# Kernel tuning notes

Measured on AMD Instinct MI355X. Metric: run time of the kernel, lower is better.

## Reference

```python
import jax, jax.numpy as jnp
import numpy as np

B, N, F_IN, F_OUT = 8, 8192, 64, 64
LN_EPS = 1e-5


def setup_inputs() -> dict:
    key = jax.random.key(0)
    k_x, k_adj, k_ws, k_wn = jax.random.split(key, 4)
    scale = 1.0 / np.sqrt(F_IN)
    return {
        "x": jax.random.normal(k_x, (B, N, F_IN), dtype=jnp.float32),
        "adj_matrix": jax.random.randint(k_adj, (N, N), 0, 2, dtype=jnp.int32),
        "W_self": jax.random.normal(k_ws, (F_IN, F_OUT), dtype=jnp.float32) * scale,
        "b_self": jnp.zeros((F_OUT,), dtype=jnp.float32),
        "W_neigh": jax.random.normal(k_wn, (F_IN, F_OUT), dtype=jnp.float32) * scale,
        "b_neigh": jnp.zeros((F_OUT,), dtype=jnp.float32),
        "ln_gamma": jnp.ones((F_OUT,), dtype=jnp.float32),
        "ln_beta": jnp.zeros((F_OUT,), dtype=jnp.float32),
    }


def reference(x, adj_matrix, W_self, b_self, W_neigh, b_neigh, ln_gamma, ln_beta):
    # GraphSAGE 'mean' conv (vectorized form of the per-node python loop):
    # agg[b,i,:] = mean over neighbors j (adj[i,j] > 0) of x[b,j,:]
    A = (adj_matrix > 0).astype(x.dtype)                 # [N, N]
    deg = A.sum(axis=1)                                  # [N]
    agg = jnp.einsum('ij,bjf->bif', A, x)                # [B, N, F_in]
    agg = agg / jnp.maximum(deg, 1.0)[None, :, None]
    neigh_out = agg @ W_neigh + b_neigh                  # [B, N, F_out]
    # nodes with no neighbors keep zeros (loop never writes them)
    neigh_out = jnp.where((deg > 0)[None, :, None], neigh_out, 0.0)
    self_out = x @ W_self + b_self                       # [B, N, F_out]
    out = jax.nn.relu(self_out + neigh_out)              # SAGE internal relu
    # GCNBlock: relu (idempotent here) -> LayerNorm; dropout is eval-mode identity
    out = jax.nn.relu(out)
    mu = out.mean(axis=-1, keepdims=True)
    var = jnp.mean((out - mu) ** 2, axis=-1, keepdims=True)
    out = (out - mu) * jax.lax.rsqrt(var + LN_EPS) * ln_gamma + ln_beta
    return out
```

## Files before the change

kernel.cpp:

```cpp
#include <hip/hip_runtime.h>

#define NN 8192

typedef __bf16 bf16x8 __attribute__((ext_vector_type(8)));
typedef float f32x4 __attribute__((ext_vector_type(4)));
typedef unsigned short u16x8 __attribute__((ext_vector_type(8)));
typedef int i32x4 __attribute__((ext_vector_type(4)));
typedef int i32x16 __attribute__((ext_vector_type(16)));

#define GLOBAL_AS __attribute__((address_space(1)))
#define LDS_AS __attribute__((address_space(3)))

__device__ __forceinline__ unsigned short f2bf(float f) {
  unsigned int u = __builtin_bit_cast(unsigned int, f);
  u += 0x7FFFu + ((u >> 16) & 1u);
  return (unsigned short)(u >> 16);
}
__device__ __forceinline__ float bf2f(unsigned short b) {
  unsigned int u = ((unsigned int)b) << 16;
  return __builtin_bit_cast(float, u);
}

__device__ __forceinline__ i32x4 expA(unsigned int h) {
  i32x4 a;
  a[0] = (int)((((h      ) & 0xFu) * 0x204081u) & 0x01010101u);
  a[1] = (int)((((h >> 4 ) & 0xFu) * 0x204081u) & 0x01010101u);
  a[2] = (int)((((h >> 8 ) & 0xFu) * 0x204081u) & 0x01010101u);
  a[3] = (int)((((h >> 12) & 0xFu) * 0x204081u) & 0x01010101u);
  return a;
}

__global__ __launch_bounds__(256) void packprep_kernel(
    const int* __restrict__ adj, unsigned long long* __restrict__ maskT,
    float* __restrict__ degp,
    const float* __restrict__ x, const float* __restrict__ Wself,
    const float* __restrict__ bself, const float* __restrict__ Wneigh,
    char* __restrict__ Yq, unsigned short* __restrict__ Sout) {
  __shared__ __align__(16) unsigned char xb[4][1024];
  __shared__ __align__(16) unsigned short xa[64 * 64];
  __shared__ __align__(16) unsigned short bm[128 * 64];

  if (blockIdx.x < 4096) {
    const int lane = threadIdx.x & 63;
    const int wv = threadIdx.x >> 6;
    const int bid = blockIdx.x;
    const int row = ((bid & 7) << 10) + ((bid >> 3) << 1) + (wv >> 1);
    const int half = wv & 1;
    const int* src = adj + (size_t)row * NN + half * 4096;
    unsigned int nib[16];
#pragma unroll
    for (int c = 0; c < 16; ++c) {
      int4 v = *(const int4*)(src + c * 256 + lane * 4);
      nib[c] = (unsigned int)(v.x > 0)
             | ((unsigned int)(v.y > 0) << 1)
             | ((unsigned int)(v.z > 0) << 2)
             | ((unsigned int)(v.w > 0) << 3);
    }
#pragma unroll
    for (int c = 0; c < 16; ++c) xb[wv][c * 64 + lane] = (unsigned char)nib[c];
    __syncthreads();
    uint4 B = *(const uint4*)&xb[wv][lane * 16];
    unsigned int t0 = (B.x | (B.x >> 4)) & 0x00FF00FFu; t0 = (t0 | (t0 >> 8)) & 0xFFFFu;
    unsigned int t1 = (B.y | (B.y >> 4)) & 0x00FF00FFu; t1 = (t1 | (t1 >> 8)) & 0xFFFFu;
    unsigned int t2 = (B.z | (B.z >> 4)) & 0x00FF00FFu; t2 = (t2 | (t2 >> 8)) & 0xFFFFu;
    unsigned int t3 = (B.w | (B.w >> 4)) & 0x00FF00FFu; t3 = (t3 | (t3 >> 8)) & 0xFFFFu;
    unsigned long long word = (unsigned long long)(t0 | (t1 << 16))
                            | ((unsigned long long)(t2 | (t3 << 16)) << 32);
    const size_t P = (size_t)((half << 5) + (lane >> 1));
    maskT[(P * NN + row) * 2 + (lane & 1)] = word;
    int deg = (int)__popcll(word);
#pragma unroll
    for (int m = 1; m < 64; m <<= 1) deg += __shfl_xor(deg, m);
    if (lane == 0) degp[half * NN + row] = (float)deg;
    return;
  }

  const int t = threadIdx.x;
  const int pb = blockIdx.x - 4096;
  const int b = pb >> 7;
  const int j0 = (pb & 127) << 6;

  {
    const float* Wsel = (t < 128) ? Wneigh : Wself;
    const int tt = t & 127;
    const int k = tt >> 1;
    const int c0 = (tt & 1) << 5;
    const int nbase = (t < 128) ? 0 : 64;
    const float4* src = (const float4*)(Wsel + k * 64 + c0);
#pragma unroll
    for (int q = 0; q < 8; ++q) {
      float4 v = src[q];
      int n0 = nbase + c0 + q * 4;
      int n;
      n = n0 + 0; bm[n * 64 + (k ^ ((n & 7) << 3))] = f2bf(v.x);
      n = n0 + 1; bm[n * 64 + (k ^ ((n & 7) << 3))] = f2bf(v.y);
      n = n0 + 2; bm[n * 64 + (k ^ ((n & 7) << 3))] = f2bf(v.z);
      n = n0 + 3; bm[n * 64 + (k ^ ((n & 7) << 3))] = f2bf(v.w);
    }
  }
  {
    const int j = t >> 2, q = t & 3;
    const float* xrow = x + ((size_t)b * NN + j0 + j) * 64 + q * 16;
    float4 v0 = *(const float4*)(xrow + 0);
    float4 v1 = *(const float4*)(xrow + 4);
    float4 v2 = *(const float4*)(xrow + 8);
    float4 v3 = *(const float4*)(xrow + 12);
    u16x8 p0, p1;
    p0[0] = f2bf(v0.x); p0[1] = f2bf(v0.y); p0[2] = f2bf(v0.z); p0[3] = f2bf(v0.w);
    p0[4] = f2bf(v1.x); p0[5] = f2bf(v1.y); p0[6] = f2bf(v1.z); p0[7] = f2bf(v1.w);
    p1[0] = f2bf(v2.x); p1[1] = f2bf(v2.y); p1[2] = f2bf(v2.z); p1[3] = f2bf(v2.w);
    p1[4] = f2bf(v3.x); p1[5] = f2bf(v3.y); p1[6] = f2bf(v3.z); p1[7] = f2bf(v3.w);
    const int base = q * 16;
    const int sw = (j & 7) << 3;
    *(u16x8*)&xa[j * 64 + (base ^ sw)] = p0;
    *(u16x8*)&xa[j * 64 + ((base + 8) ^ sw)] = p1;
  }
  __syncthreads();

  const int lane = t & 63, w = t >> 6;
  const int rl = lane & 15, hi = lane >> 4;
  f32x4 acc[8];
#pragma unroll
  for (int i = 0; i < 8; ++i) acc[i] = (f32x4){0.f, 0.f, 0.f, 0.f};

#pragma unroll
  for (int ks = 0; ks < 2; ++ks) {
    const int r = w * 16 + rl;
    const int kel = ks * 32 + hi * 8;
    bf16x8 af = __builtin_bit_cast(bf16x8, *(u16x8*)&xa[r * 64 + (kel ^ ((r & 7) << 3))]);
#pragma unroll
    for (int nf = 0; nf < 8; ++nf) {
      const int n = nf * 16 + rl;
      bf16x8 bv = __builtin_bit_cast(bf16x8, *(u16x8*)&bm[n * 64 + (kel ^ ((n & 7) << 3))]);
      acc[nf] = __builtin_amdgcn_mfma_f32_16x16x32_bf16(af, bv, acc[nf], 0, 0, 0);
    }
  }
#pragma unroll
  for (int nf = 0; nf < 8; ++nf) {
    if (nf < 4) {
      const int n = nf * 16 + rl;
      unsigned int pkt = 0;
#pragma unroll
      for (int r = 0; r < 4; ++r) {
        float v = fminf(fmaxf(acc[nf][r] * 16.0f, -127.0f), 127.0f);
        int iv = __float2int_rn(v);
        pkt |= ((unsigned int)(iv & 0xFF)) << (r * 8);
      }
      *(unsigned int*)(Yq + (size_t)(b * 64 + n) * NN + j0 + w * 16 + hi * 4) = pkt;
    } else {
      const int fo = (nf - 4) * 16 + rl;
      const float bsv = bself[fo];
#pragma unroll
      for (int r = 0; r < 4; ++r) {
        const int jj = w * 16 + hi * 4 + r;
        Sout[((size_t)b * NN + j0 + jj) * 64 + fo] = f2bf(acc[nf][r] + bsv);
      }
    }
  }
}

__global__ __launch_bounds__(256, 2) void gemm_kernel(
    const i32x4* __restrict__ mask,
    const char* __restrict__ Yq,
    unsigned short* __restrict__ Cp) {
  __shared__ __align__(16) char yL[8][8192];
  const int tid = threadIdx.x;
  const int lane = tid & 63, w = tid >> 6;
  const int nid = ((blockIdx.x & 7) << 6) + (blockIdx.x >> 3);
  const int ksp = nid >> 8;
  const int nb = (nid >> 5) & 7;
  const int mb = nid & 31;
  const int i0 = mb << 8;
  const int kbase = ksp << 12;
  const int ncol0 = nb << 6;
  const int l31 = lane & 31, l5 = lane >> 5;
  const int hs16 = l5 << 4;

  const int cst = (w << 4) + (lane >> 3);
  const char* ysrc = Yq + (size_t)(ncol0 + cst) * NN + kbase
                     + (((lane & 7) ^ (cst & 7)) << 4);
  const i32x4* mqT = mask + ((size_t)(ksp << 5)) * NN + i0 + (w << 6) + l31;

  int boff[2][4];
#pragma unroll
  for (int nf = 0; nf < 2; ++nf)
#pragma unroll
    for (int s = 0; s < 4; ++s) {
      const int col = (nf << 5) + l31;
      const int g = (s << 1) + l5;
      boff[nf][s] = (col << 7) + ((g ^ (col & 7)) << 4);
    }

  i32x16 acc[2][2];
#pragma unroll
  for (int mf = 0; mf < 2; ++mf)
#pragma unroll
    for (int nf = 0; nf < 2; ++nf)
#pragma unroll
      for (int e = 0; e < 16; ++e) acc[mf][nf][e] = 0;

#define BARRIER  __builtin_amdgcn_s_barrier()
#define MEMBAR   asm volatile("" ::: "memory")
#define WAIT_VM6 asm volatile("s_waitcnt vmcnt(6)" ::: "memory")

#define STAGE(t)                                                              \
  {                                                                           \
    __builtin_amdgcn_global_load_lds(                                         \
        (GLOBAL_AS void*)const_cast<char*>(ysrc + (size_t)((t) & 31) * 128),  \
        (LDS_AS void*)&yL[(t) & 7][w << 11], 16, 0, 0);                       \
    __builtin_amdgcn_global_load_lds(                                         \
        (GLOBAL_AS void*)const_cast<char*>(ysrc + (size_t)8 * NN              \
                                           + (size_t)((t) & 31) * 128),       \
        (LDS_AS void*)&yL[(t) & 7][(w << 11) + 1024], 16, 0, 0);              \
  }

#define LOADM(M0, M1, t)                                                      \
  { M0 = mqT[(size_t)((t) & 31) * NN]; M1 = mqT[(size_t)((t) & 31) * NN + 32]; }

#define COMPUTE(t, M0, M1)                                                    \
  {                                                                           \
    const char* yb_ = &yL[(t) & 7][0];                                        \
    __builtin_amdgcn_s_setprio(1);                                            \
    _Pragma("unroll")                                                         \
    for (int s_ = 0; s_ < 4; ++s_) {                                          \
      i32x4 b0_ = *(const i32x4*)(yb_ + boff[0][s_]);                         \
      i32x4 b1_ = *(const i32x4*)(yb_ + boff[1][s_]);                         \
      unsigned int h0_ = (unsigned int)(M0)[s_] >> hs16;                      \
      unsigned int h1_ = (unsigned int)(M1)[s_] >> hs16;                      \
      i32x4 a0_ = expA(h0_);                                                  \
      i32x4 a1_ = expA(h1_);                                                  \
      acc[0][0] = __builtin_amdgcn_mfma_i32_32x32x32_i8(a0_, b0_, acc[0][0], 0, 0, 0); \
      acc[0][1] = __builtin_amdgcn_mfma_i32_32x32x32_i8(a0_, b1_, acc[0][1], 0, 0, 0); \
      acc[1][0] = __builtin_amdgcn_mfma_i32_32x32x32_i8(a1_, b0_, acc[1][0], 0, 0, 0); \
      acc[1][1] = __builtin_amdgcn_mfma_i32_32x32x32_i8(a1_, b1_, acc[1][1], 0, 0, 0); \
    }                                                                         \
    __builtin_amdgcn_s_setprio(0);                                            \
  }

  i32x4 Ma0, Ma1, Mb0, Mb1;
  STAGE(0);
  STAGE(1);
  STAGE(2);
  LOADM(Ma0, Ma1, 0);

  for (int t2 = 0; t2 < 32; t2 += 2) {
    LOADM(Mb0, Mb1, t2 + 1);
    STAGE(t2 + 3);
    WAIT_VM6;
    BARRIER; MEMBAR;
    COMPUTE(t2, Ma0, Ma1);
    LOADM(Ma0, Ma1, t2 + 2);
    STAGE(t2 + 4);
    WAIT_VM6;
    BARRIER; MEMBAR;
    COMPUTE(t2 + 1, Mb0, Mb1);
  }
  asm volatile("s_waitcnt vmcnt(0)" ::: "memory");

#pragma unroll
  for (int mf = 0; mf < 2; ++mf)
#pragma unroll
    for (int nf = 0; nf < 2; ++nf) {
      const int col = ncol0 + (nf << 5) + l31;
#pragma unroll
      for (int r = 0; r < 16; ++r) {
        const int row = i0 + (w << 6) + (mf << 5) + (r & 3) + ((r >> 2) << 3) + (l5 << 2);
        Cp[((size_t)ksp * NN + row) * 512 + col] = f2bf((float)acc[mf][nf][r] * 0.0625f);
      }
    }
#undef BARRIER
#undef MEMBAR
#undef WAIT_VM6
#undef STAGE
#undef LOADM
#undef COMPUTE
}

__global__ __launch_bounds__(256) void epi_kernel(
    const unsigned short* __restrict__ Cp, const float* __restrict__ degp,
    const unsigned short* __restrict__ Sbf, const float* __restrict__ bneigh,
    const float* __restrict__ gamma, const float* __restrict__ beta,
    float* __restrict__ out) {
  const int lane = threadIdx.x & 63;
  const int wid = (blockIdx.x << 2) + (threadIdx.x >> 6);
  const int b = wid >> 13;
  const int i = wid & (NN - 1);
  const float deg = degp[i] + degp[NN + i];
  const float rdeg = 1.0f / fmaxf(deg, 1.0f);
  const size_t cidx = (size_t)i * 512 + b * 64 + lane;
  const float c = bf2f(Cp[cidx]) + bf2f(Cp[(size_t)NN * 512 + cidx]);
  const float sv = bf2f(Sbf[((size_t)b * NN + i) * 64 + lane]);
  float v = sv + ((deg > 0.5f) ? (c * rdeg + bneigh[lane]) : 0.0f);
  v = fmaxf(v, 0.0f);
  float s1 = v, s2 = v * v;
#pragma unroll
  for (int m = 1; m < 64; m <<= 1) {
    s1 += __shfl_xor(s1, m);
    s2 += __shfl_xor(s2, m);
  }
  const float mu = s1 * 0.015625f;
  const float var = s2 * 0.015625f - mu * mu;
  const float o = (v - mu) * rsqrtf(var + 1e-5f) * gamma[lane] + beta[lane];
  out[((size_t)b * NN + i) * 64 + lane] = o;
}

extern "C" void kernel_launch(void* const* d_in, const int* in_sizes, int n_in,
                              void* d_out, int out_size, void* d_ws, size_t ws_size,
                              hipStream_t stream) {
  (void)in_sizes; (void)n_in; (void)out_size; (void)ws_size;
  const float* x      = (const float*)d_in[0];
  const int*   adj    = (const int*)d_in[1];
  const float* Wself  = (const float*)d_in[2];
  const float* bself  = (const float*)d_in[3];
  const float* Wneigh = (const float*)d_in[4];
  const float* bneigh = (const float*)d_in[5];
  const float* gamma  = (const float*)d_in[6];
  const float* beta   = (const float*)d_in[7];
  char* ws = (char*)d_ws;
  char*               Yq    = ws;
  unsigned long long* maskT = (unsigned long long*)(ws + 4194304);
  unsigned short*     Sbf   = (unsigned short*)(ws + 12582912);
  unsigned short*     Cp    = (unsigned short*)(ws + 20971520);
  float*              degp  = (float*)(ws + 37748736);
  float*              out   = (float*)d_out;

  packprep_kernel<<<dim3(5120), dim3(256), 0, stream>>>(
      adj, maskT, degp, x, Wself, bself, Wneigh, Yq, Sbf);
  gemm_kernel<<<dim3(512), dim3(256), 0, stream>>>((const i32x4*)maskT, Yq, Cp);
  epi_kernel<<<dim3(16384), dim3(256), 0, stream>>>(Cp, degp, Sbf, bneigh, gamma, beta, out);
}
```

Measured before the change: 118.9 us.

## Split pack/prep kernels and retile int8 GEMM to smaller M tile with higher occupancy

Splits the fused pack+prep kernel into two separate launches and drops the block-wide barrier in the adjacency packing path, since each wave only reads its own LDS slice. The int8 MFMA GEMM is retiled from 256 to 128 rows per block, with half the accumulators per wave, a 4-deep LDS ring instead of 8, and launch bounds for 4 blocks per CU. The pipeline now issues the next stage after the barrier. The aim is higher occupancy and better latency hiding. In exchange, each Yq column tile is reloaded by twice as many blocks, and there is one extra kernel launch.

```diff
diff --git a/kernel.cpp b/kernel.cpp
--- a/kernel.cpp
+++ b/kernel.cpp
@@ -30,55 +30,49 @@
   return a;
 }
 
-__global__ __launch_bounds__(256) void packprep_kernel(
+__global__ __launch_bounds__(256) void pack_kernel(
     const int* __restrict__ adj, unsigned long long* __restrict__ maskT,
-    float* __restrict__ degp,
+    float* __restrict__ degp) {
+  __shared__ __align__(16) unsigned char xb[4][1024];
+  const int lane = threadIdx.x & 63;
+  const int wv = threadIdx.x >> 6;
+  const int bid = blockIdx.x;
+  const int row = ((bid & 7) << 10) + ((bid >> 3) << 1) + (wv >> 1);
+  const int half = wv & 1;
+  const int* src = adj + (size_t)row * NN + half * 4096;
+#pragma unroll
+  for (int c = 0; c < 16; ++c) {
+    int4 v = *(const int4*)(src + c * 256 + lane * 4);
+    unsigned int nib = (unsigned int)(v.x > 0)
+                     | ((unsigned int)(v.y > 0) << 1)
+                     | ((unsigned int)(v.z > 0) << 2)
+                     | ((unsigned int)(v.w > 0) << 3);
+    xb[wv][c * 64 + lane] = (unsigned char)nib;
+  }
+  uint4 B = *(const uint4*)&xb[wv][lane * 16];
+  unsigned int t0 = (B.x | (B.x >> 4)) & 0x00FF00FFu; t0 = (t0 | (t0 >> 8)) & 0xFFFFu;
+  unsigned int t1 = (B.y | (B.y >> 4)) & 0x00FF00FFu; t1 = (t1 | (t1 >> 8)) & 0xFFFFu;
+  unsigned int t2 = (B.z | (B.z >> 4)) & 0x00FF00FFu; t2 = (t2 | (t2 >> 8)) & 0xFFFFu;
+  unsigned int t3 = (B.w | (B.w >> 4)) & 0x00FF00FFu; t3 = (t3 | (t3 >> 8)) & 0xFFFFu;
+  unsigned long long word = (unsigned long long)(t0 | (t1 << 16))
+                          | ((unsigned long long)(t2 | (t3 << 16)) << 32);
+  const size_t P = (size_t)((half << 5) + (lane >> 1));
+  maskT[(P * NN + row) * 2 + (lane & 1)] = word;
+  int deg = (int)__popcll(word);
+#pragma unroll
+  for (int m = 1; m < 64; m <<= 1) deg += __shfl_xor(deg, m);
+  if (lane == 0) degp[half * NN + row] = (float)deg;
+}
+
+__global__ __launch_bounds__(256) void prep_kernel(
     const float* __restrict__ x, const float* __restrict__ Wself,
     const float* __restrict__ bself, const float* __restrict__ Wneigh,
     char* __restrict__ Yq, unsigned short* __restrict__ Sout) {
-  __shared__ __align__(16) unsigned char xb[4][1024];
   __shared__ __align__(16) unsigned short xa[64 * 64];
   __shared__ __align__(16) unsigned short bm[128 * 64];
-
-  if (blockIdx.x < 4096) {
-    const int lane = threadIdx.x & 63;
-    const int wv = threadIdx.x >> 6;
-    const int bid = blockIdx.x;
-    const int row = ((bid & 7) << 10) + ((bid >> 3) << 1) + (wv >> 1);
-    const int half = wv & 1;
-    const int* src = adj + (size_t)row * NN + half * 4096;
-    unsigned int nib[16];
-#pragma unroll
-    for (int c = 0; c < 16; ++c) {
-      int4 v = *(const int4*)(src + c * 256 + lane * 4);
-      nib[c] = (unsigned int)(v.x > 0)
-             | ((unsigned int)(v.y > 0) << 1)
-             | ((unsigned int)(v.z > 0) << 2)
-             | ((unsigned int)(v.w > 0) << 3);
-    }
-#pragma unroll
-    for (int c = 0; c < 16; ++c) xb[wv][c * 64 + lane] = (unsigned char)nib[c];
-    __syncthreads();
-    uint4 B = *(const uint4*)&xb[wv][lane * 16];
-    unsigned int t0 = (B.x | (B.x >> 4)) & 0x00FF00FFu; t0 = (t0 | (t0 >> 8)) & 0xFFFFu;
-    unsigned int t1 = (B.y | (B.y >> 4)) & 0x00FF00FFu; t1 = (t1 | (t1 >> 8)) & 0xFFFFu;
-    unsigned int t2 = (B.z | (B.z >> 4)) & 0x00FF00FFu; t2 = (t2 | (t2 >> 8)) & 0xFFFFu;
-    unsigned int t3 = (B.w | (B.w >> 4)) & 0x00FF00FFu; t3 = (t3 | (t3 >> 8)) & 0xFFFFu;
-    unsigned long long word = (unsigned long long)(t0 | (t1 << 16))
-                            | ((unsigned long long)(t2 | (t3 << 16)) << 32);
-    const size_t P = (size_t)((half << 5) + (lane >> 1));
-    maskT[(P * NN + row) * 2 + (lane & 1)] = word;
-    int deg = (int)__popcll(word);
-#pragma unroll
-    for (int m = 1; m < 64; m <<= 1) deg += __shfl_xor(deg, m);
-    if (lane == 0) degp[half * NN + row] = (float)deg;
-    return;
-  }
-
   const int t = threadIdx.x;
-  const int pb = blockIdx.x - 4096;
-  const int b = pb >> 7;
-  const int j0 = (pb & 127) << 6;
+  const int b = blockIdx.x >> 7;
+  const int j0 = (blockIdx.x & 127) << 6;
 
   {
     const float* Wsel = (t < 128) ? Wneigh : Wself;
@@ -159,18 +153,18 @@
   }
 }
 
-__global__ __launch_bounds__(256, 2) void gemm_kernel(
+__global__ __launch_bounds__(256, 4) void gemm_kernel(
     const i32x4* __restrict__ mask,
     const char* __restrict__ Yq,
     unsigned short* __restrict__ Cp) {
-  __shared__ __align__(16) char yL[8][8192];
+  __shared__ __align__(16) char yL[4][8192];
   const int tid = threadIdx.x;
   const int lane = tid & 63, w = tid >> 6;
-  const int nid = ((blockIdx.x & 7) << 6) + (blockIdx.x >> 3);
-  const int ksp = nid >> 8;
-  const int nb = (nid >> 5) & 7;
-  const int mb = nid & 31;
-  const int i0 = mb << 8;
+  const int nid = ((blockIdx.x & 7) << 7) + (blockIdx.x >> 3);
+  const int ksp = nid >> 9;
+  const int nb = (nid >> 6) & 7;
+  const int mb = nid & 63;
+  const int i0 = mb << 7;
   const int kbase = ksp << 12;
   const int ncol0 = nb << 6;
   const int l31 = lane & 31, l5 = lane >> 5;
@@ -179,7 +173,7 @@
   const int cst = (w << 4) + (lane >> 3);
   const char* ysrc = Yq + (size_t)(ncol0 + cst) * NN + kbase
                      + (((lane & 7) ^ (cst & 7)) << 4);
-  const i32x4* mqT = mask + ((size_t)(ksp << 5)) * NN + i0 + (w << 6) + l31;
+  const i32x4* mqT = mask + ((size_t)(ksp << 5)) * NN + i0 + (w << 5) + l31;
 
   int boff[2][4];
 #pragma unroll
@@ -191,13 +185,11 @@
       boff[nf][s] = (col << 7) + ((g ^ (col & 7)) << 4);
     }
 
-  i32x16 acc[2][2];
-#pragma unroll
-  for (int mf = 0; mf < 2; ++mf)
-#pragma unroll
-    for (int nf = 0; nf < 2; ++nf)
-#pragma unroll
-      for (int e = 0; e < 16; ++e) acc[mf][nf][e] = 0;
+  i32x16 acc[2];
+#pragma unroll
+  for (int nf = 0; nf < 2; ++nf)
+#pragma unroll
+    for (int e = 0; e < 16; ++e) acc[nf][e] = 0;
 
 #define BARRIER  __builtin_amdgcn_s_barrier()
 #define MEMBAR   asm volatile("" ::: "memory")
@@ -207,72 +199,62 @@
   {                                                                           \
     __builtin_amdgcn_global_load_lds(                                         \
         (GLOBAL_AS void*)const_cast<char*>(ysrc + (size_t)((t) & 31) * 128),  \
-        (LDS_AS void*)&yL[(t) & 7][w << 11], 16, 0, 0);                       \
+        (LDS_AS void*)&yL[(t) & 3][w << 11], 16, 0, 0);                       \
     __builtin_amdgcn_global_load_lds(                                         \
         (GLOBAL_AS void*)const_cast<char*>(ysrc + (size_t)8 * NN              \
                                            + (size_t)((t) & 31) * 128),       \
-        (LDS_AS void*)&yL[(t) & 7][(w << 11) + 1024], 16, 0, 0);              \
-  }
-
-#define LOADM(M0, M1, t)                                                      \
-  { M0 = mqT[(size_t)((t) & 31) * NN]; M1 = mqT[(size_t)((t) & 31) * NN + 32]; }
-
-#define COMPUTE(t, M0, M1)                                                    \
+        (LDS_AS void*)&yL[(t) & 3][(w << 11) + 1024], 16, 0, 0);              \
+  }
+
+#define COMPUTE(t, M)                                                         \
   {                                                                           \
-    const char* yb_ = &yL[(t) & 7][0];                                        \
+    const char* yb_ = &yL[(t) & 3][0];                                        \
     __builtin_amdgcn_s_setprio(1);                                            \
     _Pragma("unroll")                                                         \
     for (int s_ = 0; s_ < 4; ++s_) {                                          \
       i32x4 b0_ = *(const i32x4*)(yb_ + boff[0][s_]);                         \
       i32x4 b1_ = *(const i32x4*)(yb_ + boff[1][s_]);                         \
-      unsigned int h0_ = (unsigned int)(M0)[s_] >> hs16;                      \
-      unsigned int h1_ = (unsigned int)(M1)[s_] >> hs16;                      \
-      i32x4 a0_ = expA(h0_);                                                  \
-      i32x4 a1_ = expA(h1_);                                                  \
-      acc[0][0] = __builtin_amdgcn_mfma_i32_32x32x32_i8(a0_, b0_, acc[0][0], 0, 0, 0); \
-      acc[0][1] = __builtin_amdgcn_mfma_i32_32x32x32_i8(a0_, b1_, acc[0][1], 0, 0, 0); \
-      acc[1][0] = __builtin_amdgcn_mfma_i32_32x32x32_i8(a1_, b0_, acc[1][0], 0, 0, 0); \
-      acc[1][1] = __builtin_amdgcn_mfma_i32_32x32x32_i8(a1_, b1_, acc[1][1], 0, 0, 0); \
+      unsigned int h_ = (unsigned int)(M)[s_] >> hs16;                        \
+      i32x4 a_ = expA(h_);                                                    \
+      acc[0] = __builtin_amdgcn_mfma_i32_32x32x32_i8(a_, b0_, acc[0], 0, 0, 0); \
+      acc[1] = __builtin_amdgcn_mfma_i32_32x32x32_i8(a_, b1_, acc[1], 0, 0, 0); \
     }                                                                         \
     __builtin_amdgcn_s_setprio(0);                                            \
   }
 
-  i32x4 Ma0, Ma1, Mb0, Mb1;
+  i32x4 Ma, Mb;
   STAGE(0);
   STAGE(1);
   STAGE(2);
-  LOADM(Ma0, Ma1, 0);
+  Ma = mqT[0];
 
   for (int t2 = 0; t2 < 32; t2 += 2) {
-    LOADM(Mb0, Mb1, t2 + 1);
-    STAGE(t2 + 3);
+    Mb = mqT[(size_t)((t2 + 1) & 31) * NN];
     WAIT_VM6;
     BARRIER; MEMBAR;
-    COMPUTE(t2, Ma0, Ma1);
-    LOADM(Ma0, Ma1, t2 + 2);
-    STAGE(t2 + 4);
+    STAGE(t2 + 3);
+    COMPUTE(t2, Ma);
+    Ma = mqT[(size_t)((t2 + 2) & 31) * NN];
     WAIT_VM6;
     BARRIER; MEMBAR;
-    COMPUTE(t2 + 1, Mb0, Mb1);
+    STAGE(t2 + 4);
+    COMPUTE(t2 + 1, Mb);
   }
   asm volatile("s_waitcnt vmcnt(0)" ::: "memory");
 
 #pragma unroll
-  for (int mf = 0; mf < 2; ++mf)
-#pragma unroll
-    for (int nf = 0; nf < 2; ++nf) {
-      const int col = ncol0 + (nf << 5) + l31;
-#pragma unroll
-      for (int r = 0; r < 16; ++r) {
-        const int row = i0 + (w << 6) + (mf << 5) + (r & 3) + ((r >> 2) << 3) + (l5 << 2);
-        Cp[((size_t)ksp * NN + row) * 512 + col] = f2bf((float)acc[mf][nf][r] * 0.0625f);
-      }
-    }
+  for (int nf = 0; nf < 2; ++nf) {
+    const int col = ncol0 + (nf << 5) + l31;
+#pragma unroll
+    for (int r = 0; r < 16; ++r) {
+      const int row = i0 + (w << 5) + (r & 3) + ((r >> 2) << 3) + (l5 << 2);
+      Cp[((size_t)ksp * NN + row) * 512 + col] = f2bf((float)acc[nf][r] * 0.0625f);
+    }
+  }
 #undef BARRIER
 #undef MEMBAR
 #undef WAIT_VM6
 #undef STAGE
-#undef LOADM
 #undef COMPUTE
 }
 
@@ -324,8 +306,8 @@
   float*              degp  = (float*)(ws + 37748736);
   float*              out   = (float*)d_out;
 
-  packprep_kernel<<<dim3(5120), dim3(256), 0, stream>>>(
-      adj, maskT, degp, x, Wself, bself, Wneigh, Yq, Sbf);
-  gemm_kernel<<<dim3(512), dim3(256), 0, stream>>>((const i32x4*)maskT, Yq, Cp);
+  pack_kernel<<<dim3(4096), dim3(256), 0, stream>>>(adj, maskT, degp);
+  prep_kernel<<<dim3(1024), dim3(256), 0, stream>>>(x, Wself, bself, Wneigh, Yq, Sbf);
+  gemm_kernel<<<dim3(1024), dim3(256), 0, stream>>>((const i32x4*)maskT, Yq, Cp);
   epi_kernel<<<dim3(16384), dim3(256), 0, stream>>>(Cp, degp, Sbf, bneigh, gamma, beta, out);
 }
```

After: 122.9 us. 3.4% more time.
